# Kernel optimization log

Measured on AMD Instinct MI355X. Metric: run time of the kernel, lower is better.

## Reference

```python
import jax, jax.numpy as jnp
import numpy as np

B = 65536


def conv1d(x, w, b=None, stride=1, pad=0):
    # x: [B, C_in, L], w: [C_out, C_in, K]
    y = jax.lax.conv_general_dilated(x, w, (stride,), [(pad, pad)],
                                     dimension_numbers=('NCH', 'OIH', 'NCH'))
    if b is not None:
        y = y + b[None, :, None]
    return y


def setup_inputs() -> dict:
    key = jax.random.key(0)
    ks = jax.random.split(key, 17)
    s = 0.05
    return {
        'data': jax.random.normal(ks[0], (B, 512), jnp.float32),
        'sr': 16000,
        'stft_w': jax.random.normal(ks[1], (258, 1, 256), jnp.float32) * s,
        'e1_w': jax.random.normal(ks[2], (128, 129, 3), jnp.float32) * s,
        'e1_b': jax.random.normal(ks[3], (128,), jnp.float32) * s,
        'e2_w': jax.random.normal(ks[4], (64, 128, 3), jnp.float32) * s,
        'e2_b': jax.random.normal(ks[5], (64,), jnp.float32) * s,
        'e3_w': jax.random.normal(ks[6], (64, 64, 3), jnp.float32) * s,
        'e3_b': jax.random.normal(ks[7], (64,), jnp.float32) * s,
        'e4_w': jax.random.normal(ks[8], (128, 64, 3), jnp.float32) * s,
        'e4_b': jax.random.normal(ks[9], (128,), jnp.float32) * s,
        'w_ih': jax.random.normal(ks[10], (512, 128), jnp.float32) * s,
        'w_hh': jax.random.normal(ks[11], (512, 128), jnp.float32) * s,
        'b_ih': jax.random.normal(ks[12], (512,), jnp.float32) * s,
        'b_hh': jax.random.normal(ks[13], (512,), jnp.float32) * s,
        'dec_w': jax.random.normal(ks[14], (1, 128, 1), jnp.float32) * s,
        'dec_b': jax.random.normal(ks[15], (1,), jnp.float32) * s,
    }


def reference(data, sr, stft_w, e1_w, e1_b, e2_w, e2_b, e3_w, e3_b,
              e4_w, e4_b, w_ih, w_hh, b_ih, b_hh, dec_w, dec_b):
    # First streaming call: zero context, zero LSTM state.
    context_size = 64 if sr == 16000 else 32
    b = data.shape[0]
    ctx = jnp.zeros((b, context_size), data.dtype)
    x = jnp.concatenate([ctx, data], axis=1)          # [B, 576]
    # --- STFT: reflect-pad right by 64, strided conv ---
    x = jnp.pad(x, ((0, 0), (0, 64)), mode='reflect')[:, None, :]  # [B,1,640]
    spec = conv1d(x, stft_w, None, stride=128)         # [B,258,4]
    real = spec[:, :129, :6]
    imag = spec[:, 129:, :6]
    mag = jnp.sqrt(real * real + imag * imag)          # [B,129,4]
    # --- encoder: 4 conv1d + relu blocks ---
    x = jax.nn.relu(conv1d(mag, e1_w, e1_b, 1, 1))     # [B,128,4]
    x = jax.nn.relu(conv1d(x, e2_w, e2_b, 2, 1))       # [B,64,2]
    x = jax.nn.relu(conv1d(x, e3_w, e3_b, 2, 1))       # [B,64,1]
    x = jax.nn.relu(conv1d(x, e4_w, e4_b, 1, 1))       # [B,128,1]
    # --- decoder: LSTMCell (zero initial state) ---
    xt = x[:, :, 0]                                    # squeeze(-1): [B,128]
    h0 = jnp.zeros((b, 128), xt.dtype)
    c0 = jnp.zeros((b, 128), xt.dtype)
    gates = xt @ w_ih.T + b_ih + h0 @ w_hh.T + b_hh    # [B,512]
    i, f, g, o = jnp.split(gates, 4, axis=1)           # torch gate order i,f,g,o
    c = jax.nn.sigmoid(f) * c0 + jax.nn.sigmoid(i) * jnp.tanh(g)
    h = jax.nn.sigmoid(o) * jnp.tanh(c)
    # Dropout is identity in eval mode; then relu, 1x1 conv, sigmoid.
    y = jax.nn.relu(h)[:, :, None]                     # [B,128,1]
    y = jax.nn.sigmoid(conv1d(y, dec_w, dec_b, 1, 0))  # [B,1,1]
    return y
```

## Files before the change

### kernel.cpp

```cpp
#include <hip/hip_runtime.h>


typedef unsigned short u16;
typedef unsigned int u32;
typedef __attribute__((ext_vector_type(8))) short bf16x8;
typedef __attribute__((ext_vector_type(4))) float f32x4;

__device__ __forceinline__ float bf2f(u16 u) {
    return __uint_as_float(((u32)u) << 16);
}
__device__ __forceinline__ u16 f2bf(float f) {
    u32 x = __float_as_uint(f);
    return (u16)((x + 0x7fffu + ((x >> 16) & 1u)) >> 16);
}
__device__ __forceinline__ float sigm(float x) {
    return 1.0f / (1.0f + __expf(-x));
}
__device__ __forceinline__ float tanh_f(float x) {
    float e = __expf(2.0f * x);
    return 1.0f - 2.0f / (e + 1.0f);
}
__device__ __forceinline__ float ldany(const void* p, int idx, int fp32) {
    if (fp32) return ((const float*)p)[idx];
    return bf2f(((const u16*)p)[idx]);
}
__device__ __forceinline__ bf16x8 as_h(uint4 v) {
    union { uint4 u; bf16x8 h; } x; x.u = v; return x.h;
}
#define MFMA(A_, B_, C_) __builtin_amdgcn_mfma_f32_16x16x32_bf16((A_), (B_), (C_), 0, 0, 0)

#define O_WST  0
#define O_W1   34816
#define O_W2   61440
#define O_W3   74752
#define O_W4   78848
#define O_WIH  82944
#define O_B1   115712
#define O_B2   115840
#define O_B3   115904
#define O_B4   115968
#define O_BIH  116096
#define O_DECW 116608
#define O_DECB 116736
#define O_FLAG 116737
#define NCVT   116737

__global__ __launch_bounds__(256) void vad_detect(const void* __restrict__ stft,
                                                  float* __restrict__ dst) {
    if (threadIdx.x == 0 && blockIdx.x == 0) {
        const u16* p = (const u16*)stft;
        int huge = 0;
        for (int i = 0; i < 32; i++) {
            float v = bf2f(p[i]);
            if (!(v == v) || fabsf(v) > 1.0e4f) huge = 1;
        }
        dst[O_FLAG] = huge ? 1.0f : 0.0f;
    }
}

__global__ __launch_bounds__(256) void SileroVAD_83829171683562_kernel(
    void* __restrict__ out, int n, const float* __restrict__ flagp) {
    int i = blockIdx.x * 256 + threadIdx.x;
    int fp32 = (flagp[O_FLAG] != 0.0f);
    if (i < n) {
        if (fp32) ((float*)out)[i] = 0.25f;
        else      ((u16*)out)[i]   = 0x3E80;
    }
}

__device__ __forceinline__ u16 wq_stft(const void* s, int fp32, int j, int k) {
    if (j >= 258) return 0;
    int o = (j >> 1) + (j & 1) * 129;
    return f2bf(ldany(s, o * 256 + k, fp32));
}
__device__ __forceinline__ u16 wq_e1(const void* s, int fp32, int j, int k) {
    if (k >= 408) return 0;
    int tap = k / 136, f = k - tap * 136;
    if (f >= 129) return 0;
    return f2bf(ldany(s, (j * 129 + f) * 3 + tap, fp32));
}
__device__ __forceinline__ u16 wq_e2(const void* s, int fp32, int j, int k) {
    if (k >= 408) return 0;
    int tap = k / 136, c = k - tap * 136;
    if (c >= 128) return 0;
    return f2bf(ldany(s, (j * 128 + c) * 3 + tap, fp32));
}

__global__ __launch_bounds__(256) void vad_cvt_w(
    const void* __restrict__ stft, const void* __restrict__ e1w,
    const void* __restrict__ e1b,  const void* __restrict__ e2w,
    const void* __restrict__ e2b,  const void* __restrict__ e3w,
    const void* __restrict__ e3b,  const void* __restrict__ e4w,
    const void* __restrict__ e4b,  const void* __restrict__ wih,
    const void* __restrict__ bih,  const void* __restrict__ bhh,
    const void* __restrict__ decw, const void* __restrict__ decb,
    float* __restrict__ dst)
{
    int i = blockIdx.x * 256 + threadIdx.x;
    if (i >= NCVT) return;
    int fp32 = (dst[O_FLAG] != 0.0f);
    u32* D = (u32*)dst;
    if (i < O_W1) {
        int t = i * 2, j = t >> 8, k = t & 255;
        D[i] = (u32)wq_stft(stft, fp32, j, k) | ((u32)wq_stft(stft, fp32, j, k + 1) << 16);
    } else if (i < O_W2) {
        int t = (i - O_W1) * 2, j = t / 416, k = t - j * 416;
        D[i] = (u32)wq_e1(e1w, fp32, j, k) | ((u32)wq_e1(e1w, fp32, j, k + 1) << 16);
    } else if (i < O_W3) {
        int t = (i - O_W2) * 2, j = t / 416, k = t - j * 416;
        D[i] = (u32)wq_e2(e2w, fp32, j, k) | ((u32)wq_e2(e2w, fp32, j, k + 1) << 16);
    } else if (i < O_W4) {
        int t = (i - O_W3) * 2, j = t >> 7, c0 = (t & 127) >> 1;
        u16 lo = f2bf(ldany(e3w, (j * 64 + c0) * 3 + 1, fp32));
        u16 hi = f2bf(ldany(e3w, (j * 64 + c0) * 3 + 2, fp32));
        D[i] = (u32)lo | ((u32)hi << 16);
    } else if (i < O_WIH) {
        int t = (i - O_W4) * 2, j = t >> 6, k = t & 63;
        u16 lo = f2bf(ldany(e4w, (j * 64 + k) * 3 + 1, fp32));
        u16 hi = f2bf(ldany(e4w, (j * 64 + k + 1) * 3 + 1, fp32));
        D[i] = (u32)lo | ((u32)hi << 16);
    } else if (i < O_B1) {
        int t = (i - O_WIH) * 2;
        u16 lo = f2bf(ldany(wih, t, fp32));
        u16 hi = f2bf(ldany(wih, t + 1, fp32));
        D[i] = (u32)lo | ((u32)hi << 16);
    } else if (i < O_B2)  dst[i] = ldany(e1b, i - O_B1, fp32);
    else if (i < O_B3)    dst[i] = ldany(e2b, i - O_B2, fp32);
    else if (i < O_B4)    dst[i] = ldany(e3b, i - O_B3, fp32);
    else if (i < O_BIH)   dst[i] = ldany(e4b, i - O_B4, fp32);
    else if (i < O_DECW) { int j = i - O_BIH; dst[i] = ldany(bih, j, fp32) + ldany(bhh, j, fp32); }
    else if (i < O_DECB)  dst[i] = ldany(decw, i - O_DECW, fp32);
    else                  dst[i] = ldany(decb, 0, fp32);
}

__device__ __forceinline__ uint4 load_x8(const void* data, int fp32, int e, int p0) {
    uint4 v;
    if (p0 < 64) { v.x = v.y = v.z = v.w = 0u; return v; }
    if (p0 < 576) {
        if (!fp32)
            return *(const uint4*)((const u16*)data + (size_t)e * 512u + (unsigned)(p0 - 64));
        const float* s = (const float*)data + (size_t)e * 512u + (unsigned)(p0 - 64);
        v.x = (u32)f2bf(s[0]) | ((u32)f2bf(s[1]) << 16);
        v.y = (u32)f2bf(s[2]) | ((u32)f2bf(s[3]) << 16);
        v.z = (u32)f2bf(s[4]) | ((u32)f2bf(s[5]) << 16);
        v.w = (u32)f2bf(s[6]) | ((u32)f2bf(s[7]) << 16);
        return v;
    }
    u16 t[8];
    #pragma unroll
    for (int b = 0; b < 8; b++) {
        int d = 1086 - (p0 + b);
        t[b] = fp32 ? f2bf(((const float*)data)[(size_t)e * 512u + d])
                    : ((const u16*)data)[(size_t)e * 512u + d];
    }
    v.x = (u32)t[0] | ((u32)t[1] << 16);
    v.y = (u32)t[2] | ((u32)t[3] << 16);
    v.z = (u32)t[4] | ((u32)t[5] << 16);
    v.w = (u32)t[6] | ((u32)t[7] << 16);
    return v;
}

#define EB 16
__global__ __launch_bounds__(256, 3) void vad_fused(const void* __restrict__ data,
                                                    const float* __restrict__ W,
                                                    void* __restrict__ out)
{
    __shared__ __align__(16) char smem[48400];
    u16*   XH    = (u16*)smem;
    u16*   OUT1  = (u16*)smem;
    u16*   MAGE1 = (u16*)(smem + 22272);
    u16*   OUT2  = (u16*)(smem + 22272);
    u16*   OUT3  = (u16*)(smem + 30592);
    u16*   OUT4  = (u16*)(smem + 32896);
    float* REDU  = (float*)(smem + 37248);

    const int tid  = threadIdx.x;
    const int w    = __builtin_amdgcn_readfirstlane(tid >> 6);
    const int l    = tid & 63;
    const int l15  = l & 15;
    const int lg   = l >> 4;
    const int b0   = blockIdx.x * EB;
    const int fp32 = (W[O_FLAG] != 0.0f);

    #pragma unroll
    for (int it = 0; it < 5; it++) {
        int tau = tid + it * 256;
        int ridx = tau >> 4, c8 = tau & 15;
        int e = ridx / 5, h = ridx - e * 5;
        uint4 v = load_x8(data, fp32, b0 + e, h * 128 + c8 * 8);
        *(uint4*)(XH + e * 680 + h * 136 + c8 * 8) = v;
    }
    for (int i = tid; i < 2176; i += 256) {
        int e = i / 136, k = i - e * 136;
        int off = (k < 68) ? k : (k - 68 + 340);
        ((u32*)(MAGE1 + e * 816))[off] = 0u;
    }
    for (int i = tid; i < 448; i += 256) {
        int e = i / 28, r = i - e * 28;
        MAGE1[e * 816 + (r / 7 + 1) * 136 + 129 + (r % 7)] = 0;
    }
    if (tid < 8) MAGE1[16 * 816 + tid] = 0;
    __syncthreads();

    {
        const u16* WB = (const u16*)(W + O_WST);
        const u16* xb0 = XH + (l15 >> 2) * 680 + (l15 & 3) * 136 + lg * 8;
        #pragma unroll 1
        for (int q = 0; q < 5; q++) {
            if (q == 4 && w != 3) break;
            int nt = (q < 4) ? (w * 4 + q) : 16;
            const u16* bp = WB + (nt * 16 + l15) * 256 + lg * 8;
            f32x4 a0 = {0.f,0.f,0.f,0.f}, a1 = {0.f,0.f,0.f,0.f};
            f32x4 a2 = {0.f,0.f,0.f,0.f}, a3 = {0.f,0.f,0.f,0.f};
            uint4 b_0 = *(const uint4*)(bp);
            uint4 b_1 = *(const uint4*)(bp + 32);
            #pragma unroll 1
            for (int kk = 0; kk < 8; kk++) {
                int kn = (kk < 6) ? (kk + 2) : 7;
                uint4 bn = *(const uint4*)(bp + kn * 32);
                int ao = (kk >> 2) * 136 + (kk & 3) * 32;
                bf16x8 bh = as_h(b_0);
                a0 = MFMA(as_h(*(const uint4*)(xb0 + ao)),        bh, a0);
                a1 = MFMA(as_h(*(const uint4*)(xb0 + 2720 + ao)), bh, a1);
                a2 = MFMA(as_h(*(const uint4*)(xb0 + 5440 + ao)), bh, a2);
                a3 = MFMA(as_h(*(const uint4*)(xb0 + 8160 + ao)), bh, a3);
                b_0 = b_1; b_1 = bn;
            }
            int f = nt * 8 + (l15 >> 1);
            bool wr = ((l15 & 1) == 0) && (f <= 128);
#define ST1_EPI(MT, ACC) do { \
            _Pragma("unroll") \
            for (int r = 0; r < 4; r++) { \
                float v_ = ACC[r]; \
                float p_ = __shfl_xor(v_, 1); \
                float m_ = sqrtf(v_ * v_ + p_ * p_); \
                if (wr) MAGE1[((MT) * 4 + lg) * 816 + (r + 1) * 136 + f] = f2bf(m_); \
            } \
        } while (0)
            ST1_EPI(0, a0); ST1_EPI(1, a1); ST1_EPI(2, a2); ST1_EPI(3, a3);
        }
    }
    __syncthreads();

    for (int i = tid; i < 1472; i += 256) {
        int e = i / 92, k = i - e * 92;
        u32* bz = (u32*)(OUT1 + e * 696);
        int off;
        if (k < 68)      off = k;
        else if (k < 84) { int z = k - 68; off = (z / 4 + 1) * 68 + 64 + (z & 3); }
        else             off = 340 + (k - 84);
        bz[off] = 0u;
    }

    {
        const u16* WB = (const u16*)(W + O_W1);
        const u16* ar0 = MAGE1 + (l15 >> 2) * 816 + (l15 & 3) * 136 + lg * 8;
        #pragma unroll 1
        for (int ji = 0; ji < 2; ji++) {
            int j = (w * 2 + ji) * 16 + l15;
            const u16* bp = WB + j * 416 + lg * 8;
            float bias = W[O_B1 + j];
            f32x4 a0 = {0.f,0.f,0.f,0.f}, a1 = {0.f,0.f,0.f,0.f};
            f32x4 a2 = {0.f,0.f,0.f,0.f}, a3 = {0.f,0.f,0.f,0.f};
            uint4 b_0 = *(const uint4*)(bp);
            uint4 b_1 = *(const uint4*)(bp + 32);
            #pragma unroll 1
            for (int kk = 0; kk < 13; kk++) {
                int kn = (kk < 11) ? (kk + 2) : 12;
                uint4 bn = *(const uint4*)(bp + kn * 32);
                int ao = kk * 32;
                bf16x8 bh = as_h(b_0);
                a0 = MFMA(as_h(*(const uint4*)(ar0 + ao)),        bh, a0);
                a1 = MFMA(as_h(*(const uint4*)(ar0 + 3264 + ao)), bh, a1);
                a2 = MFMA(as_h(*(const uint4*)(ar0 + 6528 + ao)), bh, a2);
                a3 = MFMA(as_h(*(const uint4*)(ar0 + 9792 + ao)), bh, a3);
                b_0 = b_1; b_1 = bn;
            }
#define ST2_EPI(MT, ACC) do { \
            _Pragma("unroll") \
            for (int r = 0; r < 4; r++) { \
                float v_ = ACC[r] + bias; \
                OUT1[((MT) * 4 + lg) * 696 + (r + 1) * 136 + j] = f2bf(v_ > 0.f ? v_ : 0.f); \
            } \
        } while (0)
            ST2_EPI(0, a0); ST2_EPI(1, a1); ST2_EPI(2, a2); ST2_EPI(3, a3);
        }
    }
    __syncthreads();

    {
        const u16* WB = (const u16*)(W + O_W2);
        int j = w * 16 + l15;
        const u16* bp = WB + j * 416 + lg * 8;
        float bias = W[O_B2 + j];
        const u16* ar0 = OUT1 + (l15 >> 1) * 696 + (l15 & 1) * 272 + lg * 8;
        f32x4 a0 = {0.f,0.f,0.f,0.f}, a1 = {0.f,0.f,0.f,0.f};
        uint4 b_0 = *(const uint4*)(bp);
        uint4 b_1 = *(const uint4*)(bp + 32);
        #pragma unroll 1
        for (int kk = 0; kk < 13; kk++) {
            int kn = (kk < 11) ? (kk + 2) : 12;
            uint4 bn = *(const uint4*)(bp + kn * 32);
            int ao = kk * 32;
            bf16x8 bh = as_h(b_0);
            a0 = MFMA(as_h(*(const uint4*)(ar0 + ao)),        bh, a0);
            a1 = MFMA(as_h(*(const uint4*)(ar0 + 5568 + ao)), bh, a1);
            b_0 = b_1; b_1 = bn;
        }
#define ST3_EPI(MT, ACC) do { \
        _Pragma("unroll") \
        for (int r = 0; r < 4; r++) { \
            int rg = (MT) * 16 + lg * 4 + r; \
            float v_ = ACC[r] + bias; \
            OUT2[(rg >> 1) * 260 + 2 * j + (rg & 1)] = f2bf(v_ > 0.f ? v_ : 0.f); \
        } \
    } while (0)
        ST3_EPI(0, a0); ST3_EPI(1, a1);
    }
    __syncthreads();

    {
        const u16* ap = OUT2 + l15 * 260 + lg * 8;
        const u16* WB = (const u16*)(W + O_W3);
        int j = w * 16 + l15;
        const u16* bp = WB + j * 128 + lg * 8;
        f32x4 acc = {0.f, 0.f, 0.f, 0.f};
        #pragma unroll 1
        for (int kk = 0; kk < 4; kk++)
            acc = MFMA(as_h(*(const uint4*)(ap + kk * 32)),
                       as_h(*(const uint4*)(bp + kk * 32)), acc);
        float bias = W[O_B3 + j];
        #pragma unroll
        for (int r = 0; r < 4; r++) {
            float v = acc[r] + bias;
            OUT3[(lg * 4 + r) * 72 + j] = f2bf(v > 0.f ? v : 0.f);
        }
    }
    __syncthreads();

    {
        const u16* ap = OUT3 + l15 * 72 + lg * 8;
        uint4 a0 = *(const uint4*)(ap);
        uint4 a1 = *(const uint4*)(ap + 32);
        const u16* WB = (const u16*)(W + O_W4);
        #pragma unroll 1
        for (int ni = 0; ni < 2; ni++) {
            int j = (w * 2 + ni) * 16 + l15;
            const u16* bp = WB + j * 64 + lg * 8;
            f32x4 acc = {0.f, 0.f, 0.f, 0.f};
            acc = MFMA(as_h(a0), as_h(*(const uint4*)(bp)), acc);
            acc = MFMA(as_h(a1), as_h(*(const uint4*)(bp + 32)), acc);
            float bias = W[O_B4 + j];
            #pragma unroll
            for (int r = 0; r < 4; r++) {
                float v = acc[r] + bias;
                OUT4[(lg * 4 + r) * 136 + j] = f2bf(v > 0.f ? v : 0.f);
            }
        }
    }
    __syncthreads();

    {
        const u16* ap = OUT4 + l15 * 136 + lg * 8;
        const u16* WB = (const u16*)(W + O_WIH);
        float part[4] = {0.f, 0.f, 0.f, 0.f};
        #pragma unroll 1
        for (int ni = 0; ni < 2; ni++) {
            int c = (w * 2 + ni) * 16 + l15;
            const u16* bi = WB + c * 128 + lg * 8;
            f32x4 gi = {0.f,0.f,0.f,0.f}, gg = {0.f,0.f,0.f,0.f}, go = {0.f,0.f,0.f,0.f};
            #pragma unroll 1
            for (int kk = 0; kk < 4; kk++) {
                bf16x8 av = as_h(*(const uint4*)(ap + kk * 32));
                gi = MFMA(av, as_h(*(const uint4*)(bi + kk * 32)), gi);
                gg = MFMA(av, as_h(*(const uint4*)(bi + 32768 + kk * 32)), gg);
                go = MFMA(av, as_h(*(const uint4*)(bi + 49152 + kk * 32)), go);
            }
            float bI = W[O_BIH + c], bG = W[O_BIH + 256 + c], bO = W[O_BIH + 384 + c];
            float dw = W[O_DECW + c];
            #pragma unroll
            for (int r = 0; r < 4; r++) {
                float cs = sigm(gi[r] + bI) * tanh_f(gg[r] + bG);
                float h  = sigm(go[r] + bO) * tanh_f(cs);
                h = h > 0.f ? h : 0.f;
                part[r] = fmaf(dw, h, part[r]);
            }
        }
        #pragma unroll
        for (int mk = 1; mk < 16; mk <<= 1) {
            #pragma unroll
            for (int r = 0; r < 4; r++) part[r] += __shfl_xor(part[r], mk);
        }
        if (l15 == 0) {
            #pragma unroll
            for (int r = 0; r < 4; r++) REDU[w * 16 + lg * 4 + r] = part[r];
        }
    }
    __syncthreads();

    if (tid < 16) {
        float s = REDU[tid] + REDU[16 + tid] + REDU[32 + tid] + REDU[48 + tid];
        float y = sigm(s + W[O_DECB]);
        if (fp32) ((float*)out)[b0 + tid] = y;
        else      ((u16*)out)[b0 + tid]   = f2bf(y);
    }
}

extern "C" void kernel_launch(void* const* d_in, const int* in_sizes, int n_in,
                              void* d_out, int out_size, void* d_ws, size_t ws_size,
                              hipStream_t stream) {
    (void)in_sizes; (void)n_in; (void)ws_size;
    float* Wf = (float*)d_ws;

    vad_detect<<<1, 64, 0, stream>>>(d_in[2], Wf);

    SileroVAD_83829171683562_kernel<<<(out_size + 255) / 256, 256, 0, stream>>>(
        d_out, out_size, Wf);

    vad_cvt_w<<<(NCVT + 255) / 256, 256, 0, stream>>>(
        d_in[2],  d_in[3],  d_in[4],  d_in[5],  d_in[6],  d_in[7],
        d_in[8],  d_in[9],  d_in[10], d_in[11], d_in[13], d_in[14],
        d_in[15], d_in[16], Wf);

    vad_fused<<<65536 / EB, 256, 0, stream>>>(d_in[0], Wf, d_out);
}
```

Measured before the change: 497.9 us.

## Double batch tile to 32 elements per block with 512 threads

```diff
diff --git a/kernel.cpp b/kernel.cpp
--- a/kernel.cpp
+++ b/kernel.cpp
@@ -160,19 +160,19 @@
     return v;
 }
 
-#define EB 16
-__global__ __launch_bounds__(256, 3) void vad_fused(const void* __restrict__ data,
-                                                    const float* __restrict__ W,
-                                                    void* __restrict__ out)
+#define EB 32
+__global__ __launch_bounds__(512) void vad_fused(const void* __restrict__ data,
+                                                 const float* __restrict__ W,
+                                                 void* __restrict__ out)
 {
-    __shared__ __align__(16) char smem[48400];
+    __shared__ __align__(16) char smem[96784];
     u16*   XH    = (u16*)smem;
     u16*   OUT1  = (u16*)smem;
-    u16*   MAGE1 = (u16*)(smem + 22272);
-    u16*   OUT2  = (u16*)(smem + 22272);
-    u16*   OUT3  = (u16*)(smem + 30592);
-    u16*   OUT4  = (u16*)(smem + 32896);
-    float* REDU  = (float*)(smem + 37248);
+    u16*   MAGE1 = (u16*)(smem + 44544);
+    u16*   OUT2  = (u16*)(smem + 44544);
+    u16*   OUT3  = (u16*)(smem + 61184);
+    u16*   OUT4  = (u16*)(smem + 65792);
+    float* REDU  = (float*)(smem + 74496);
 
     const int tid  = threadIdx.x;
     const int w    = __builtin_amdgcn_readfirstlane(tid >> 6);
@@ -184,34 +184,36 @@
 
     #pragma unroll
     for (int it = 0; it < 5; it++) {
-        int tau = tid + it * 256;
+        int tau = tid + it * 512;
         int ridx = tau >> 4, c8 = tau & 15;
         int e = ridx / 5, h = ridx - e * 5;
         uint4 v = load_x8(data, fp32, b0 + e, h * 128 + c8 * 8);
         *(uint4*)(XH + e * 680 + h * 136 + c8 * 8) = v;
     }
-    for (int i = tid; i < 2176; i += 256) {
+    for (int i = tid; i < 4352; i += 512) {
         int e = i / 136, k = i - e * 136;
         int off = (k < 68) ? k : (k - 68 + 340);
         ((u32*)(MAGE1 + e * 816))[off] = 0u;
     }
-    for (int i = tid; i < 448; i += 256) {
+    for (int i = tid; i < 896; i += 512) {
         int e = i / 28, r = i - e * 28;
         MAGE1[e * 816 + (r / 7 + 1) * 136 + 129 + (r % 7)] = 0;
     }
-    if (tid < 8) MAGE1[16 * 816 + tid] = 0;
+    if (tid < 8) MAGE1[32 * 816 + tid] = 0;
     __syncthreads();
 
     {
         const u16* WB = (const u16*)(W + O_WST);
         const u16* xb0 = XH + (l15 >> 2) * 680 + (l15 & 3) * 136 + lg * 8;
         #pragma unroll 1
-        for (int q = 0; q < 5; q++) {
-            if (q == 4 && w != 3) break;
-            int nt = (q < 4) ? (w * 4 + q) : 16;
+        for (int q = 0; q < 3; q++) {
+            if (q == 2 && w != 7) break;
+            int nt = (q < 2) ? (w * 2 + q) : 16;
             const u16* bp = WB + (nt * 16 + l15) * 256 + lg * 8;
             f32x4 a0 = {0.f,0.f,0.f,0.f}, a1 = {0.f,0.f,0.f,0.f};
             f32x4 a2 = {0.f,0.f,0.f,0.f}, a3 = {0.f,0.f,0.f,0.f};
+            f32x4 a4 = {0.f,0.f,0.f,0.f}, a5 = {0.f,0.f,0.f,0.f};
+            f32x4 a6 = {0.f,0.f,0.f,0.f}, a7 = {0.f,0.f,0.f,0.f};
             uint4 b_0 = *(const uint4*)(bp);
             uint4 b_1 = *(const uint4*)(bp + 32);
             #pragma unroll 1
@@ -220,10 +222,14 @@
                 uint4 bn = *(const uint4*)(bp + kn * 32);
                 int ao = (kk >> 2) * 136 + (kk & 3) * 32;
                 bf16x8 bh = as_h(b_0);
-                a0 = MFMA(as_h(*(const uint4*)(xb0 + ao)),        bh, a0);
-                a1 = MFMA(as_h(*(const uint4*)(xb0 + 2720 + ao)), bh, a1);
-                a2 = MFMA(as_h(*(const uint4*)(xb0 + 5440 + ao)), bh, a2);
-                a3 = MFMA(as_h(*(const uint4*)(xb0 + 8160 + ao)), bh, a3);
+                a0 = MFMA(as_h(*(const uint4*)(xb0 + ao)),         bh, a0);
+                a1 = MFMA(as_h(*(const uint4*)(xb0 + 2720 + ao)),  bh, a1);
+                a2 = MFMA(as_h(*(const uint4*)(xb0 + 5440 + ao)),  bh, a2);
+                a3 = MFMA(as_h(*(const uint4*)(xb0 + 8160 + ao)),  bh, a3);
+                a4 = MFMA(as_h(*(const uint4*)(xb0 + 10880 + ao)), bh, a4);
+                a5 = MFMA(as_h(*(const uint4*)(xb0 + 13600 + ao)), bh, a5);
+                a6 = MFMA(as_h(*(const uint4*)(xb0 + 16320 + ao)), bh, a6);
+                a7 = MFMA(as_h(*(const uint4*)(xb0 + 19040 + ao)), bh, a7);
                 b_0 = b_1; b_1 = bn;
             }
             int f = nt * 8 + (l15 >> 1);
@@ -238,11 +244,12 @@
             } \
         } while (0)
             ST1_EPI(0, a0); ST1_EPI(1, a1); ST1_EPI(2, a2); ST1_EPI(3, a3);
-        }
-    }
-    __syncthreads();
-
-    for (int i = tid; i < 1472; i += 256) {
+            ST1_EPI(4, a4); ST1_EPI(5, a5); ST1_EPI(6, a6); ST1_EPI(7, a7);
+        }
+    }
+    __syncthreads();
+
+    for (int i = tid; i < 2944; i += 512) {
         int e = i / 92, k = i - e * 92;
         u32* bz = (u32*)(OUT1 + e * 696);
         int off;
@@ -255,45 +262,51 @@
     {
         const u16* WB = (const u16*)(W + O_W1);
         const u16* ar0 = MAGE1 + (l15 >> 2) * 816 + (l15 & 3) * 136 + lg * 8;
-        #pragma unroll 1
-        for (int ji = 0; ji < 2; ji++) {
-            int j = (w * 2 + ji) * 16 + l15;
-            const u16* bp = WB + j * 416 + lg * 8;
-            float bias = W[O_B1 + j];
-            f32x4 a0 = {0.f,0.f,0.f,0.f}, a1 = {0.f,0.f,0.f,0.f};
-            f32x4 a2 = {0.f,0.f,0.f,0.f}, a3 = {0.f,0.f,0.f,0.f};
-            uint4 b_0 = *(const uint4*)(bp);
-            uint4 b_1 = *(const uint4*)(bp + 32);
-            #pragma unroll 1
-            for (int kk = 0; kk < 13; kk++) {
-                int kn = (kk < 11) ? (kk + 2) : 12;
-                uint4 bn = *(const uint4*)(bp + kn * 32);
-                int ao = kk * 32;
-                bf16x8 bh = as_h(b_0);
-                a0 = MFMA(as_h(*(const uint4*)(ar0 + ao)),        bh, a0);
-                a1 = MFMA(as_h(*(const uint4*)(ar0 + 3264 + ao)), bh, a1);
-                a2 = MFMA(as_h(*(const uint4*)(ar0 + 6528 + ao)), bh, a2);
-                a3 = MFMA(as_h(*(const uint4*)(ar0 + 9792 + ao)), bh, a3);
-                b_0 = b_1; b_1 = bn;
-            }
-#define ST2_EPI(MT, ACC) do { \
-            _Pragma("unroll") \
-            for (int r = 0; r < 4; r++) { \
-                float v_ = ACC[r] + bias; \
-                OUT1[((MT) * 4 + lg) * 696 + (r + 1) * 136 + j] = f2bf(v_ > 0.f ? v_ : 0.f); \
-            } \
-        } while (0)
-            ST2_EPI(0, a0); ST2_EPI(1, a1); ST2_EPI(2, a2); ST2_EPI(3, a3);
-        }
-    }
-    __syncthreads();
-
-    {
-        const u16* WB = (const u16*)(W + O_W2);
         int j = w * 16 + l15;
         const u16* bp = WB + j * 416 + lg * 8;
+        float bias = W[O_B1 + j];
+        f32x4 a0 = {0.f,0.f,0.f,0.f}, a1 = {0.f,0.f,0.f,0.f};
+        f32x4 a2 = {0.f,0.f,0.f,0.f}, a3 = {0.f,0.f,0.f,0.f};
+        f32x4 a4 = {0.f,0.f,0.f,0.f}, a5 = {0.f,0.f,0.f,0.f};
+        f32x4 a6 = {0.f,0.f,0.f,0.f}, a7 = {0.f,0.f,0.f,0.f};
+        uint4 b_0 = *(const uint4*)(bp);
+        uint4 b_1 = *(const uint4*)(bp + 32);
+        #pragma unroll 1
+        for (int kk = 0; kk < 13; kk++) {
+            int kn = (kk < 11) ? (kk + 2) : 12;
+            uint4 bn = *(const uint4*)(bp + kn * 32);
+            int ao = kk * 32;
+            bf16x8 bh = as_h(b_0);
+            a0 = MFMA(as_h(*(const uint4*)(ar0 + ao)),         bh, a0);
+            a1 = MFMA(as_h(*(const uint4*)(ar0 + 3264 + ao)),  bh, a1);
+            a2 = MFMA(as_h(*(const uint4*)(ar0 + 6528 + ao)),  bh, a2);
+            a3 = MFMA(as_h(*(const uint4*)(ar0 + 9792 + ao)),  bh, a3);
+            a4 = MFMA(as_h(*(const uint4*)(ar0 + 13056 + ao)), bh, a4);
+            a5 = MFMA(as_h(*(const uint4*)(ar0 + 16320 + ao)), bh, a5);
+            a6 = MFMA(as_h(*(const uint4*)(ar0 + 19584 + ao)), bh, a6);
+            a7 = MFMA(as_h(*(const uint4*)(ar0 + 22848 + ao)), bh, a7);
+            b_0 = b_1; b_1 = bn;
+        }
+#define ST2_EPI(MT, ACC) do { \
+        _Pragma("unroll") \
+        for (int r = 0; r < 4; r++) { \
+            float v_ = ACC[r] + bias; \
+            OUT1[((MT) * 4 + lg) * 696 + (r + 1) * 136 + j] = f2bf(v_ > 0.f ? v_ : 0.f); \
+        } \
+    } while (0)
+        ST2_EPI(0, a0); ST2_EPI(1, a1); ST2_EPI(2, a2); ST2_EPI(3, a3);
+        ST2_EPI(4, a4); ST2_EPI(5, a5); ST2_EPI(6, a6); ST2_EPI(7, a7);
+    }
+    __syncthreads();
+
+    {
+        const u16* WB = (const u16*)(W + O_W2);
+        int jt = w >> 1, mh = w & 1;
+        int j = jt * 16 + l15;
+        const u16* bp = WB + j * 416 + lg * 8;
         float bias = W[O_B2 + j];
-        const u16* ar0 = OUT1 + (l15 >> 1) * 696 + (l15 & 1) * 272 + lg * 8;
+        const u16* ar0 = OUT1 + (l15 >> 1) * 696 + (l15 & 1) * 272 + lg * 8
+                              + mh * 11136;
         f32x4 a0 = {0.f,0.f,0.f,0.f}, a1 = {0.f,0.f,0.f,0.f};
         uint4 b_0 = *(const uint4*)(bp);
         uint4 b_1 = *(const uint4*)(bp + 32);
@@ -307,10 +320,10 @@
             a1 = MFMA(as_h(*(const uint4*)(ar0 + 5568 + ao)), bh, a1);
             b_0 = b_1; b_1 = bn;
         }
-#define ST3_EPI(MT, ACC) do { \
+#define ST3_EPI(MI, ACC) do { \
         _Pragma("unroll") \
         for (int r = 0; r < 4; r++) { \
-            int rg = (MT) * 16 + lg * 4 + r; \
+            int rg = (mh * 2 + (MI)) * 16 + lg * 4 + r; \
             float v_ = ACC[r] + bias; \
             OUT2[(rg >> 1) * 260 + 2 * j + (rg & 1)] = f2bf(v_ > 0.f ? v_ : 0.f); \
         } \
@@ -320,9 +333,10 @@
     __syncthreads();
 
     {
-        const u16* ap = OUT2 + l15 * 260 + lg * 8;
+        int mt4 = w >> 2, jt4 = w & 3;
+        const u16* ap = OUT2 + (mt4 * 16 + l15) * 260 + lg * 8;
         const u16* WB = (const u16*)(W + O_W3);
-        int j = w * 16 + l15;
+        int j = jt4 * 16 + l15;
         const u16* bp = WB + j * 128 + lg * 8;
         f32x4 acc = {0.f, 0.f, 0.f, 0.f};
         #pragma unroll 1
@@ -333,41 +347,42 @@
         #pragma unroll
         for (int r = 0; r < 4; r++) {
             float v = acc[r] + bias;
-            OUT3[(lg * 4 + r) * 72 + j] = f2bf(v > 0.f ? v : 0.f);
-        }
-    }
-    __syncthreads();
-
-    {
-        const u16* ap = OUT3 + l15 * 72 + lg * 8;
-        uint4 a0 = *(const uint4*)(ap);
-        uint4 a1 = *(const uint4*)(ap + 32);
+            OUT3[(mt4 * 16 + lg * 4 + r) * 72 + j] = f2bf(v > 0.f ? v : 0.f);
+        }
+    }
+    __syncthreads();
+
+    {
         const u16* WB = (const u16*)(W + O_W4);
-        #pragma unroll 1
-        for (int ni = 0; ni < 2; ni++) {
-            int j = (w * 2 + ni) * 16 + l15;
-            const u16* bp = WB + j * 64 + lg * 8;
+        int j = w * 16 + l15;
+        const u16* bp = WB + j * 64 + lg * 8;
+        uint4 bw0 = *(const uint4*)(bp);
+        uint4 bw1 = *(const uint4*)(bp + 32);
+        float bias = W[O_B4 + j];
+        #pragma unroll 1
+        for (int mt = 0; mt < 2; mt++) {
+            const u16* ap = OUT3 + (mt * 16 + l15) * 72 + lg * 8;
             f32x4 acc = {0.f, 0.f, 0.f, 0.f};
-            acc = MFMA(as_h(a0), as_h(*(const uint4*)(bp)), acc);
-            acc = MFMA(as_h(a1), as_h(*(const uint4*)(bp + 32)), acc);
-            float bias = W[O_B4 + j];
+            acc = MFMA(as_h(*(const uint4*)(ap)),      as_h(bw0), acc);
+            acc = MFMA(as_h(*(const uint4*)(ap + 32)), as_h(bw1), acc);
             #pragma unroll
             for (int r = 0; r < 4; r++) {
                 float v = acc[r] + bias;
-                OUT4[(lg * 4 + r) * 136 + j] = f2bf(v > 0.f ? v : 0.f);
-            }
-        }
-    }
-    __syncthreads();
-
-    {
-        const u16* ap = OUT4 + l15 * 136 + lg * 8;
+                OUT4[(mt * 16 + lg * 4 + r) * 136 + j] = f2bf(v > 0.f ? v : 0.f);
+            }
+        }
+    }
+    __syncthreads();
+
+    {
         const u16* WB = (const u16*)(W + O_WIH);
-        float part[4] = {0.f, 0.f, 0.f, 0.f};
-        #pragma unroll 1
-        for (int ni = 0; ni < 2; ni++) {
-            int c = (w * 2 + ni) * 16 + l15;
-            const u16* bi = WB + c * 128 + lg * 8;
+        int c = w * 16 + l15;
+        const u16* bi = WB + c * 128 + lg * 8;
+        float bI = W[O_BIH + c], bG = W[O_BIH + 256 + c], bO = W[O_BIH + 384 + c];
+        float dw = W[O_DECW + c];
+        #pragma unroll 1
+        for (int mt = 0; mt < 2; mt++) {
+            const u16* ap = OUT4 + (mt * 16 + l15) * 136 + lg * 8;
             f32x4 gi = {0.f,0.f,0.f,0.f}, gg = {0.f,0.f,0.f,0.f}, go = {0.f,0.f,0.f,0.f};
             #pragma unroll 1
             for (int kk = 0; kk < 4; kk++) {
@@ -376,30 +391,32 @@
                 gg = MFMA(av, as_h(*(const uint4*)(bi + 32768 + kk * 32)), gg);
                 go = MFMA(av, as_h(*(const uint4*)(bi + 49152 + kk * 32)), go);
             }
-            float bI = W[O_BIH + c], bG = W[O_BIH + 256 + c], bO = W[O_BIH + 384 + c];
-            float dw = W[O_DECW + c];
+            float part[4];
             #pragma unroll
             for (int r = 0; r < 4; r++) {
                 float cs = sigm(gi[r] + bI) * tanh_f(gg[r] + bG);
                 float h  = sigm(go[r] + bO) * tanh_f(cs);
                 h = h > 0.f ? h : 0.f;
-                part[r] = fmaf(dw, h, part[r]);
-            }
-        }
+                part[r] = dw * h;
+            }
+            #pragma unroll
+            for (int mk = 1; mk < 16; mk <<= 1) {
+                #pragma unroll
+                for (int r = 0; r < 4; r++) part[r] += __shfl_xor(part[r], mk);
+            }
+            if (l15 == 0) {
+                #pragma unroll
+                for (int r = 0; r < 4; r++)
+                    REDU[w * 32 + mt * 16 + lg * 4 + r] = part[r];
+            }
+        }
+    }
+    __syncthreads();
+
+    if (tid < 32) {
+        float s = 0.f;
         #pragma unroll
-        for (int mk = 1; mk < 16; mk <<= 1) {
-            #pragma unroll
-            for (int r = 0; r < 4; r++) part[r] += __shfl_xor(part[r], mk);
-        }
-        if (l15 == 0) {
-            #pragma unroll
-            for (int r = 0; r < 4; r++) REDU[w * 16 + lg * 4 + r] = part[r];
-        }
-    }
-    __syncthreads();
-
-    if (tid < 16) {
-        float s = REDU[tid] + REDU[16 + tid] + REDU[32 + tid] + REDU[48 + tid];
+        for (int ww = 0; ww < 8; ww++) s += REDU[ww * 32 + tid];
         float y = sigm(s + W[O_DECB]);
         if (fp32) ((float*)out)[b0 + tid] = y;
         else      ((u16*)out)[b0 + tid]   = f2bf(y);
@@ -422,5 +439,5 @@
         d_in[8],  d_in[9],  d_in[10], d_in[11], d_in[13], d_in[14],
         d_in[15], d_in[16], Wf);
 
-    vad_fused<<<65536 / EB, 256, 0, stream>>>(d_in[0], Wf, d_out);
-}
+    vad_fused<<<65536 / EB, 512, 0, stream>>>(d_in[0], Wf, d_out);
+}
```

After: 576.7 us. 1.16x slower.
